# Kernel tuning notes

Measured on AMD Instinct MI355X. Metric: run time of the kernel, lower is better.

## Reference

```python
import jax, jax.numpy as jnp
import numpy as np

N_NODES = 100000
N_EDGES = 1600000


def setup_inputs() -> dict:
    key = jax.random.key(0)
    ks = jax.random.split(key, 6)
    x = jax.random.normal(ks[0], (N_NODES, 128), dtype=jnp.float32)
    src = jax.random.randint(ks[1], (N_EDGES,), 0, N_NODES, dtype=jnp.int32)
    dst = jax.random.randint(ks[2], (N_EDGES,), 0, N_NODES, dtype=jnp.int32)
    # Glorot-ish scaled weights
    W1 = jax.random.normal(ks[3], (128, 64), dtype=jnp.float32) / np.sqrt(128.0)
    b1 = jnp.zeros((64,), dtype=jnp.float32)
    W2 = jax.random.normal(ks[4], (64, 64), dtype=jnp.float32) / np.sqrt(64.0)
    b2 = jnp.zeros((64,), dtype=jnp.float32)
    return {"x": x, "src": src, "dst": dst, "W1": W1, "b1": b1, "W2": W2, "b2": b2}


def _gcn_forward(x, src_f, dst_f, norm_src, norm_dst, W1, b1, W2, b2):
    n = x.shape[0]

    def conv(h, W, b):
        # weight-first (in_feats >= out_feats in DGL GraphConv): h W is cheap, aggregate small dim
        h = h @ W                                  # [N, d_out]
        h = h * norm_src[:, None]                  # D_out^{-1/2} on source side
        msg = h[src_f]                             # gather per edge [E+N, d_out]
        agg = jax.ops.segment_sum(msg, dst_f, num_segments=n)  # scatter-add to dst
        return agg * norm_dst[:, None] + b         # D_in^{-1/2} + bias

    h = jax.nn.relu(conv(x, W1, b1))
    return conv(h, W2, b2)


def reference(x, src, dst, W1, b1, W2, b2):
    n = x.shape[0]
    loop = jnp.arange(n, dtype=src.dtype)
    src_f = jnp.concatenate([src, loop])  # dgl.add_self_loop
    dst_f = jnp.concatenate([dst, loop])
    ones = jnp.ones(src_f.shape[0], dtype=x.dtype)
    out_deg = jax.ops.segment_sum(ones, src_f, num_segments=n)
    in_deg = jax.ops.segment_sum(ones, dst_f, num_segments=n)
    norm_src = jax.lax.rsqrt(out_deg)  # deg >= 1 due to self loops
    norm_dst = jax.lax.rsqrt(in_deg)
    return _gcn_forward(x, src_f, dst_f, norm_src, norm_dst, W1, b1, W2, b2)
```

## Files before the change

kernel.cpp:

```cpp
#include <hip/hip_runtime.h>
#include <hip/hip_fp16.h>

#define D 64
#define SLICE 25000
#define NBUCK 512
#define EPB 4096

typedef __attribute__((ext_vector_type(8))) short short8;
typedef __attribute__((ext_vector_type(4))) float floatx4;

__global__ __launch_bounds__(256) void k_hist(const int* __restrict__ src,
                                              const int* __restrict__ dst,
                                              int* __restrict__ cnt_out,
                                              int* __restrict__ cnt_in,
                                              int E, int N) {
    __shared__ int h[SLICE];
    const int* idx = blockIdx.z ? dst : src;
    int* cnt       = blockIdx.z ? cnt_in : cnt_out;
    int lo = blockIdx.y * SLICE;
    int hi = min(lo + SLICE, N);
    int len = hi - lo;
    for (int i = threadIdx.x; i < len; i += 256) h[i] = 0;
    __syncthreads();

    const int E4 = E >> 2;
    const int4* idx4 = (const int4*)idx;
    int stride = gridDim.x * 256;
    for (int i = blockIdx.x * 256 + threadIdx.x; i < E4; i += stride) {
        int4 v = idx4[i];
        if (v.x >= lo && v.x < hi) atomicAdd(&h[v.x - lo], 1);
        if (v.y >= lo && v.y < hi) atomicAdd(&h[v.y - lo], 1);
        if (v.z >= lo && v.z < hi) atomicAdd(&h[v.z - lo], 1);
        if (v.w >= lo && v.w < hi) atomicAdd(&h[v.w - lo], 1);
    }
    if (blockIdx.x == 0) {
        int e = E4 * 4 + threadIdx.x;
        if (e < E) {
            int v = idx[e];
            if (v >= lo && v < hi) atomicAdd(&h[v - lo], 1);
        }
    }
    __syncthreads();
    for (int i = threadIdx.x; i < len; i += 256) {
        int c = h[i];
        if (c) atomicAdd(&cnt[lo + i], c);
    }
}

__global__ __launch_bounds__(256) void k_norm(const int* __restrict__ cnt,
                                              float* __restrict__ nrm, int n) {
    int i = blockIdx.x * 256 + threadIdx.x;
    if (i < n) nrm[i] = rsqrtf((float)cnt[i] + 1.0f);
}

__global__ __launch_bounds__(256) void k_scan1(const int* __restrict__ in,
                                               int* __restrict__ out,
                                               int* __restrict__ partials, int n) {
    __shared__ int s[256];
    int tid = threadIdx.x;
    int base = blockIdx.x * 1024 + tid * 4;
    int v[4];
#pragma unroll
    for (int j = 0; j < 4; ++j) v[j] = (base + j < n) ? in[base + j] : 0;
    int l1 = v[0] + v[1];
    int l2 = l1 + v[2];
    int total = l2 + v[3];
    s[tid] = total;
    __syncthreads();
    for (int off = 1; off < 256; off <<= 1) {
        int add = (tid >= off) ? s[tid - off] : 0;
        __syncthreads();
        s[tid] += add;
        __syncthreads();
    }
    int excl = s[tid] - total;
    if (base + 0 < n) out[base + 0] = excl;
    if (base + 1 < n) out[base + 1] = excl + v[0];
    if (base + 2 < n) out[base + 2] = excl + l1;
    if (base + 3 < n) out[base + 3] = excl + l2;
    if (tid == 255) partials[blockIdx.x] = s[255];
}

__global__ void k_scan2(int* __restrict__ partials, int B) {
    if (threadIdx.x == 0) {
        int run = 0;
        for (int i = 0; i < B; ++i) {
            int tmp = partials[i];
            partials[i] = run;
            run += tmp;
        }
    }
}

__global__ __launch_bounds__(256) void k_scan3(int* __restrict__ out,
                                               const int* __restrict__ partials, int n) {
    int off = partials[blockIdx.x];
    int base = blockIdx.x * 1024 + threadIdx.x * 4;
#pragma unroll
    for (int j = 0; j < 4; ++j)
        if (base + j < n) out[base + j] += off;
}

__global__ __launch_bounds__(256) void k_bhist(const int* __restrict__ dst,
                                               int* __restrict__ bucket_cnt, int E) {
    __shared__ int h[NBUCK];
    for (int i = threadIdx.x; i < NBUCK; i += 256) h[i] = 0;
    __syncthreads();
    const int E4 = E >> 2;
    const int4* d4 = (const int4*)dst;
    int stride = gridDim.x * 256;
    for (int i = blockIdx.x * 256 + threadIdx.x; i < E4; i += stride) {
        int4 v = d4[i];
        atomicAdd(&h[v.x >> 8], 1);
        atomicAdd(&h[v.y >> 8], 1);
        atomicAdd(&h[v.z >> 8], 1);
        atomicAdd(&h[v.w >> 8], 1);
    }
    if (blockIdx.x == 0) {
        int e = E4 * 4 + threadIdx.x;
        if (e < E) atomicAdd(&h[dst[e] >> 8], 1);
    }
    __syncthreads();
    for (int i = threadIdx.x; i < NBUCK; i += 256) {
        int c = h[i];
        if (c) atomicAdd(&bucket_cnt[i], c);
    }
}

__global__ __launch_bounds__(256) void k_bscan(const int* __restrict__ bucket_cnt,
                                               int* __restrict__ bucket_base) {
    __shared__ int s[256];
    int tid = threadIdx.x;
    int a = bucket_cnt[2 * tid];
    int b = bucket_cnt[2 * tid + 1];
    s[tid] = a + b;
    __syncthreads();
    for (int off = 1; off < 256; off <<= 1) {
        int add = (tid >= off) ? s[tid - off] : 0;
        __syncthreads();
        s[tid] += add;
        __syncthreads();
    }
    int excl = s[tid] - (a + b);
    bucket_base[2 * tid]     = excl;
    bucket_base[2 * tid + 1] = excl + a;
}

__global__ __launch_bounds__(256) void k_bin(const int* __restrict__ src,
                                             const int* __restrict__ dst,
                                             const int* __restrict__ bucket_base,
                                             int* __restrict__ bucket_cursor,
                                             unsigned long long* __restrict__ binned,
                                             int E) {
    __shared__ int cnt[NBUCK];
    __shared__ int bloc[NBUCK];
    __shared__ int lcur[NBUCK];
    __shared__ int gbase[NBUCK];
    __shared__ int ss[256];
    __shared__ unsigned long long stage[EPB];

    int tid = threadIdx.x;
    int start = blockIdx.x * EPB;
    int nloc = min(EPB, E - start);

    for (int i = tid; i < NBUCK; i += 256) cnt[i] = 0;
    __syncthreads();

#pragma unroll
    for (int r = 0; r < EPB / 256; ++r) {
        int idx = start + r * 256 + tid;
        if (idx < E) atomicAdd(&cnt[dst[idx] >> 8], 1);
    }
    __syncthreads();

    int a = cnt[2 * tid], b = cnt[2 * tid + 1];
    ss[tid] = a + b;
    __syncthreads();
    for (int off = 1; off < 256; off <<= 1) {
        int add = (tid >= off) ? ss[tid - off] : 0;
        __syncthreads();
        ss[tid] += add;
        __syncthreads();
    }
    int excl = ss[tid] - (a + b);
    bloc[2 * tid] = excl;           lcur[2 * tid] = excl;
    bloc[2 * tid + 1] = excl + a;   lcur[2 * tid + 1] = excl + a;
    __syncthreads();

    for (int bk = tid; bk < NBUCK; bk += 256) {
        int c = cnt[bk];
        gbase[bk] = c ? (atomicAdd(&bucket_cursor[bk], c) + bucket_base[bk]) : 0;
    }
    __syncthreads();

#pragma unroll
    for (int r = 0; r < EPB / 256; ++r) {
        int idx = start + r * 256 + tid;
        if (idx < E) {
            int d = dst[idx];
            int p = atomicAdd(&lcur[d >> 8], 1);
            stage[p] = ((unsigned long long)(unsigned)d << 32) | (unsigned)src[idx];
        }
    }
    __syncthreads();

#pragma unroll
    for (int r = 0; r < EPB / 256; ++r) {
        int i = r * 256 + tid;
        if (i < nloc) {
            unsigned long long e = stage[i];
            int bk = (int)(e >> 40);
            binned[gbase[bk] + (i - bloc[bk])] = e;
        }
    }
}

__global__ __launch_bounds__(256) void k_bsort(const unsigned long long* __restrict__ binned,
                                               const int* __restrict__ bucket_base,
                                               const int* __restrict__ bucket_cnt,
                                               const int* __restrict__ row_ptr,
                                               int* __restrict__ csr, int N) {
    __shared__ int cur[256];
    int b = blockIdx.x;
    int n0 = b << 8;
    int tid = threadIdx.x;
    if (n0 + tid < N) cur[tid] = row_ptr[n0 + tid];
    __syncthreads();
    int base = bucket_base[b];
    int c = bucket_cnt[b];
    for (int k = tid; k < c; k += 256) {
        unsigned long long e = binned[base + k];
        int d = (int)(e >> 32);
        int s = (int)(e & 0xffffffffu);
        int p = atomicAdd(&cur[d - n0], 1);
        csr[p] = s;
    }
}

template <int K>
__global__ __launch_bounds__(256) void k_gemm_mfma(const float* __restrict__ hsrc,
                                                   const float* __restrict__ W,
                                                   const float* __restrict__ norm_src,
                                                   __half* __restrict__ t, int N) {
    constexpr int NKI = K / 32;
    __shared__ short Whi[NKI * 2048];
    __shared__ short Wlo[NKI * 2048];
    int tid = threadIdx.x;

    for (int f = tid; f < K * 64; f += 256) {
        int n  = f & 15;
        int j  = (f >> 4) & 7;
        int q  = (f >> 7) & 3;
        int ct = (f >> 9) & 3;
        int ki = f >> 11;
        int k = ki * 32 + q * 8 + j;
        int c = ct * 16 + n;
        float w = W[k * 64 + c];
        unsigned u = __float_as_uint(w);
        float l = w - __uint_as_float(u & 0xffff0000u);
        int idx = (((ki * 4 + ct) * 16 + n) * 4 + q) * 8 + j;
        Whi[idx] = (short)(u >> 16);
        Wlo[idx] = (short)(__float_as_uint(l) >> 16);
    }
    __syncthreads();

    int wave = tid >> 6, lane = tid & 63;
    int q = lane >> 4, n = lane & 15;
    int r0 = blockIdx.x * 64 + wave * 16;
    int rowc = min(r0 + n, N - 1);

    floatx4 acc[4] = {{0.f,0.f,0.f,0.f},{0.f,0.f,0.f,0.f},
                      {0.f,0.f,0.f,0.f},{0.f,0.f,0.f,0.f}};

    for (int ki = 0; ki < NKI; ++ki) {
        const float* ap = hsrc + (long long)rowc * K + ki * 32 + q * 8;
        float4 a0 = *(const float4*)ap;
        float4 a1 = *(const float4*)(ap + 4);
        float av[8] = {a0.x, a0.y, a0.z, a0.w, a1.x, a1.y, a1.z, a1.w};
        short8 ahi, alo;
#pragma unroll
        for (int j = 0; j < 8; ++j) {
            unsigned u = __float_as_uint(av[j]);
            float l = av[j] - __uint_as_float(u & 0xffff0000u);
            ahi[j] = (short)(u >> 16);
            alo[j] = (short)(__float_as_uint(l) >> 16);
        }
#pragma unroll
        for (int ct = 0; ct < 4; ++ct) {
            int bidx = (((ki * 4 + ct) * 16 + n) * 4 + q) * 8;
            short8 bhi = *(const short8*)&Whi[bidx];
            short8 blo = *(const short8*)&Wlo[bidx];
            acc[ct] = __builtin_amdgcn_mfma_f32_16x16x32_bf16(ahi, bhi, acc[ct], 0, 0, 0);
            acc[ct] = __builtin_amdgcn_mfma_f32_16x16x32_bf16(ahi, blo, acc[ct], 0, 0, 0);
            acc[ct] = __builtin_amdgcn_mfma_f32_16x16x32_bf16(alo, bhi, acc[ct], 0, 0, 0);
        }
    }

#pragma unroll
    for (int reg = 0; reg < 4; ++reg) {
        int orow = r0 + q * 4 + reg;
        if (orow < N) {
            float nrm = norm_src[orow];
#pragma unroll
            for (int ct = 0; ct < 4; ++ct)
                t[(long long)orow * 64 + ct * 16 + n] = __float2half(acc[ct][reg] * nrm);
        }
    }
}

__global__ __launch_bounds__(256) void k_agg(const int* __restrict__ row_ptr,
                                             const int* __restrict__ cnt,
                                             const int* __restrict__ csr,
                                             const __half* __restrict__ t,
                                             const float* __restrict__ norm_dst,
                                             const float* __restrict__ bias,
                                             float* __restrict__ out, int N, int do_relu) {
    int tid = threadIdx.x;
    int half_id = tid >> 5;
    int lane = tid & 31;
    int i = blockIdx.x * 8 + half_id;
    if (i >= N) return;
    const __half2* t2 = (const __half2*)t;
    int start = row_ptr[i], c = cnt[i];

    __half2 self = t2[i * 32 + lane];
    float2 sf = __half22float2(self);
    float ax = sf.x, ay = sf.y;

    int j = 0;
    int pre = min(c, (4 - (start & 3)) & 3);
    for (; j < pre; ++j) {
        float2 f = __half22float2(t2[csr[start + j] * 32 + lane]);
        ax += f.x; ay += f.y;
    }
    for (; j + 4 <= c; j += 4) {
        int4 s4 = *(const int4*)&csr[start + j];
        float2 f0 = __half22float2(t2[s4.x * 32 + lane]);
        float2 f1 = __half22float2(t2[s4.y * 32 + lane]);
        float2 f2 = __half22float2(t2[s4.z * 32 + lane]);
        float2 f3 = __half22float2(t2[s4.w * 32 + lane]);
        ax += (f0.x + f1.x) + (f2.x + f3.x);
        ay += (f0.y + f1.y) + (f2.y + f3.y);
    }
    for (; j < c; ++j) {
        float2 f = __half22float2(t2[csr[start + j] * 32 + lane]);
        ax += f.x; ay += f.y;
    }

    float nrm = norm_dst[i];
    float2 bb = ((const float2*)bias)[lane];
    float vx = fmaf(ax, nrm, bb.x);
    float vy = fmaf(ay, nrm, bb.y);
    if (do_relu) { vx = fmaxf(vx, 0.f); vy = fmaxf(vy, 0.f); }
    float2 o; o.x = vx; o.y = vy;
    ((float2*)out)[i * 32 + lane] = o;
}

extern "C" void kernel_launch(void* const* d_in, const int* in_sizes, int n_in,
                              void* d_out, int out_size, void* d_ws, size_t ws_size,
                              hipStream_t stream) {
    const float* x   = (const float*)d_in[0];
    const int*   src = (const int*)d_in[1];
    const int*   dst = (const int*)d_in[2];
    const float* W1  = (const float*)d_in[3];
    const float* b1  = (const float*)d_in[4];
    const float* W2  = (const float*)d_in[5];
    const float* b2  = (const float*)d_in[6];
    float* out = (float*)d_out;

    const int N = in_sizes[0] / 128;
    const int E = in_sizes[1];

    int*   cnt_out  = (int*)d_ws;
    int*   cnt_in   = cnt_out + N;
    int*   unused0  = cnt_in + N;
    int*   row_ptr  = unused0 + N;
    int*   partials = row_ptr + N;
    float* norm_src = (float*)(partials + 1024);
    float* norm_dst = norm_src + N;
    float* tbase    = norm_dst + N;
    float* h        = tbase + (long long)N * D;
    int*   csr      = (int*)(h + (long long)N * D);
    int*   bucket_cnt    = csr + E;
    int*   bucket_cursor = bucket_cnt + NBUCK;
    int*   bucket_base   = bucket_cursor + NBUCK;
    __half* t_h = (__half*)tbase;
    unsigned long long* binned = (unsigned long long*)tbase;

    const int B = (N + 1023) / 1024;
    const int NS = (N + SLICE - 1) / SLICE;
    const int NB = (N + 255) / 256;
    const int NBK = (E + EPB - 1) / EPB;

    hipMemsetAsync(cnt_out, 0, (size_t)2 * N * sizeof(int), stream);
    hipMemsetAsync(bucket_cnt, 0, (size_t)2 * NBUCK * sizeof(int), stream);

    k_hist<<<dim3(32, NS, 2), 256, 0, stream>>>(src, dst, cnt_out, cnt_in, E, N);
    k_norm<<<(2 * N + 255) / 256, 256, 0, stream>>>(cnt_out, norm_src, 2 * N);

    k_scan1<<<B, 256, 0, stream>>>(cnt_in, row_ptr, partials, N);
    k_scan2<<<1, 64, 0, stream>>>(partials, B);
    k_scan3<<<B, 256, 0, stream>>>(row_ptr, partials, N);

    k_bhist<<<64, 256, 0, stream>>>(dst, bucket_cnt, E);
    k_bscan<<<1, 256, 0, stream>>>(bucket_cnt, bucket_base);
    k_bin<<<NBK, 256, 0, stream>>>(src, dst, bucket_base, bucket_cursor, binned, E);
    k_bsort<<<NB, 256, 0, stream>>>(binned, bucket_base, bucket_cnt, row_ptr, csr, N);

    k_gemm_mfma<128><<<(N + 63) / 64, 256, 0, stream>>>(x, W1, norm_src, t_h, N);
    k_agg<<<(N + 7) / 8, 256, 0, stream>>>(row_ptr, cnt_in, csr, t_h, norm_dst, b1, h, N, 1);

    k_gemm_mfma<64><<<(N + 63) / 64, 256, 0, stream>>>(h, W2, norm_src, t_h, N);
    k_agg<<<(N + 7) / 8, 256, 0, stream>>>(row_ptr, cnt_in, csr, t_h, norm_dst, b2, out, N, 0);
}
```

Baseline: 336.6 us.

## Split feature table into column panels and derive buckets from row_ptr

The GEMM output is now written as four 16-column panels, each N×16 in half precision, about 3.2MB per panel. Aggregation runs four passes, one per panel, with 8 lanes per node, so each pass's gathers hit a working set small enough to stay in L2/MALL instead of thrashing the whole 12.8MB table. Separately, the bucket histogram and bucket scan kernels are removed and bucket bases and counts are read from row_ptr[bucket*256], which saves two launches and a full pass over dst. In exchange the CSR indices and row metadata are re-read four times per layer, and each gather now fetches only 32 bytes per node row.

```diff
diff --git a/kernel.cpp b/kernel.cpp
--- a/kernel.cpp
+++ b/kernel.cpp
@@ -81,7 +81,8 @@
     if (tid == 255) partials[blockIdx.x] = s[255];
 }
 
-__global__ void k_scan2(int* __restrict__ partials, int B) {
+__global__ void k_scan2(int* __restrict__ partials, int B,
+                        int* __restrict__ row_ptr, int N, int E) {
     if (threadIdx.x == 0) {
         int run = 0;
         for (int i = 0; i < B; ++i) {
@@ -90,6 +91,7 @@
             run += tmp;
         }
     }
+    if (threadIdx.x == 1) row_ptr[N] = E;
 }
 
 __global__ __launch_bounds__(256) void k_scan3(int* __restrict__ out,
@@ -101,54 +103,9 @@
         if (base + j < n) out[base + j] += off;
 }
 
-__global__ __launch_bounds__(256) void k_bhist(const int* __restrict__ dst,
-                                               int* __restrict__ bucket_cnt, int E) {
-    __shared__ int h[NBUCK];
-    for (int i = threadIdx.x; i < NBUCK; i += 256) h[i] = 0;
-    __syncthreads();
-    const int E4 = E >> 2;
-    const int4* d4 = (const int4*)dst;
-    int stride = gridDim.x * 256;
-    for (int i = blockIdx.x * 256 + threadIdx.x; i < E4; i += stride) {
-        int4 v = d4[i];
-        atomicAdd(&h[v.x >> 8], 1);
-        atomicAdd(&h[v.y >> 8], 1);
-        atomicAdd(&h[v.z >> 8], 1);
-        atomicAdd(&h[v.w >> 8], 1);
-    }
-    if (blockIdx.x == 0) {
-        int e = E4 * 4 + threadIdx.x;
-        if (e < E) atomicAdd(&h[dst[e] >> 8], 1);
-    }
-    __syncthreads();
-    for (int i = threadIdx.x; i < NBUCK; i += 256) {
-        int c = h[i];
-        if (c) atomicAdd(&bucket_cnt[i], c);
-    }
-}
-
-__global__ __launch_bounds__(256) void k_bscan(const int* __restrict__ bucket_cnt,
-                                               int* __restrict__ bucket_base) {
-    __shared__ int s[256];
-    int tid = threadIdx.x;
-    int a = bucket_cnt[2 * tid];
-    int b = bucket_cnt[2 * tid + 1];
-    s[tid] = a + b;
-    __syncthreads();
-    for (int off = 1; off < 256; off <<= 1) {
-        int add = (tid >= off) ? s[tid - off] : 0;
-        __syncthreads();
-        s[tid] += add;
-        __syncthreads();
-    }
-    int excl = s[tid] - (a + b);
-    bucket_base[2 * tid]     = excl;
-    bucket_base[2 * tid + 1] = excl + a;
-}
-
 __global__ __launch_bounds__(256) void k_bin(const int* __restrict__ src,
                                              const int* __restrict__ dst,
-                                             const int* __restrict__ bucket_base,
+                                             const int* __restrict__ row_ptr,
                                              int* __restrict__ bucket_cursor,
                                              unsigned long long* __restrict__ binned,
                                              int E) {
@@ -189,7 +146,7 @@
 
     for (int bk = tid; bk < NBUCK; bk += 256) {
         int c = cnt[bk];
-        gbase[bk] = c ? (atomicAdd(&bucket_cursor[bk], c) + bucket_base[bk]) : 0;
+        gbase[bk] = c ? (atomicAdd(&bucket_cursor[bk], c) + row_ptr[bk << 8]) : 0;
     }
     __syncthreads();
 
@@ -216,8 +173,6 @@
 }
 
 __global__ __launch_bounds__(256) void k_bsort(const unsigned long long* __restrict__ binned,
-                                               const int* __restrict__ bucket_base,
-                                               const int* __restrict__ bucket_cnt,
                                                const int* __restrict__ row_ptr,
                                                int* __restrict__ csr, int N) {
     __shared__ int cur[256];
@@ -226,8 +181,8 @@
     int tid = threadIdx.x;
     if (n0 + tid < N) cur[tid] = row_ptr[n0 + tid];
     __syncthreads();
-    int base = bucket_base[b];
-    int c = bucket_cnt[b];
+    int base = row_ptr[n0];
+    int c = row_ptr[min(n0 + 256, N)] - base;
     for (int k = tid; k < c; k += 256) {
         unsigned long long e = binned[base + k];
         int d = (int)(e >> 32);
@@ -303,7 +258,7 @@
             float nrm = norm_src[orow];
 #pragma unroll
             for (int ct = 0; ct < 4; ++ct)
-                t[(long long)orow * 64 + ct * 16 + n] = __float2half(acc[ct][reg] * nrm);
+                t[(long long)ct * N * 16 + orow * 16 + n] = __float2half(acc[ct][reg] * nrm);
         }
     }
 }
@@ -311,49 +266,48 @@
 __global__ __launch_bounds__(256) void k_agg(const int* __restrict__ row_ptr,
                                              const int* __restrict__ cnt,
                                              const int* __restrict__ csr,
-                                             const __half* __restrict__ t,
+                                             const __half* __restrict__ tp,
                                              const float* __restrict__ norm_dst,
-                                             const float* __restrict__ bias,
-                                             float* __restrict__ out, int N, int do_relu) {
-    int tid = threadIdx.x;
-    int half_id = tid >> 5;
-    int lane = tid & 31;
-    int i = blockIdx.x * 8 + half_id;
+                                             const float* __restrict__ bias16,
+                                             float* __restrict__ outp,
+                                             int N, int do_relu) {
+    int tid = threadIdx.x;
+    int g = tid & 7;
+    int i = blockIdx.x * 32 + (tid >> 3);
     if (i >= N) return;
-    const __half2* t2 = (const __half2*)t;
+    const __half2* t2 = (const __half2*)tp;
     int start = row_ptr[i], c = cnt[i];
 
-    __half2 self = t2[i * 32 + lane];
-    float2 sf = __half22float2(self);
+    float2 sf = __half22float2(t2[i * 8 + g]);
     float ax = sf.x, ay = sf.y;
 
     int j = 0;
     int pre = min(c, (4 - (start & 3)) & 3);
     for (; j < pre; ++j) {
-        float2 f = __half22float2(t2[csr[start + j] * 32 + lane]);
+        float2 f = __half22float2(t2[csr[start + j] * 8 + g]);
         ax += f.x; ay += f.y;
     }
     for (; j + 4 <= c; j += 4) {
         int4 s4 = *(const int4*)&csr[start + j];
-        float2 f0 = __half22float2(t2[s4.x * 32 + lane]);
-        float2 f1 = __half22float2(t2[s4.y * 32 + lane]);
-        float2 f2 = __half22float2(t2[s4.z * 32 + lane]);
-        float2 f3 = __half22float2(t2[s4.w * 32 + lane]);
+        float2 f0 = __half22float2(t2[s4.x * 8 + g]);
+        float2 f1 = __half22float2(t2[s4.y * 8 + g]);
+        float2 f2 = __half22float2(t2[s4.z * 8 + g]);
+        float2 f3 = __half22float2(t2[s4.w * 8 + g]);
         ax += (f0.x + f1.x) + (f2.x + f3.x);
         ay += (f0.y + f1.y) + (f2.y + f3.y);
     }
     for (; j < c; ++j) {
-        float2 f = __half22float2(t2[csr[start + j] * 32 + lane]);
+        float2 f = __half22float2(t2[csr[start + j] * 8 + g]);
         ax += f.x; ay += f.y;
     }
 
     float nrm = norm_dst[i];
-    float2 bb = ((const float2*)bias)[lane];
+    float2 bb = ((const float2*)bias16)[g];
     float vx = fmaf(ax, nrm, bb.x);
     float vy = fmaf(ay, nrm, bb.y);
     if (do_relu) { vx = fmaxf(vx, 0.f); vy = fmaxf(vy, 0.f); }
     float2 o; o.x = vx; o.y = vy;
-    ((float2*)out)[i * 32 + lane] = o;
+    ((float2*)outp)[i * 32 + g] = o;
 }
 
 extern "C" void kernel_launch(void* const* d_in, const int* in_sizes, int n_in,
@@ -373,17 +327,14 @@
 
     int*   cnt_out  = (int*)d_ws;
     int*   cnt_in   = cnt_out + N;
-    int*   unused0  = cnt_in + N;
-    int*   row_ptr  = unused0 + N;
-    int*   partials = row_ptr + N;
+    int*   row_ptr  = cnt_in + N;
+    int*   partials = row_ptr + N + 1;
     float* norm_src = (float*)(partials + 1024);
     float* norm_dst = norm_src + N;
     float* tbase    = norm_dst + N;
     float* h        = tbase + (long long)N * D;
     int*   csr      = (int*)(h + (long long)N * D);
-    int*   bucket_cnt    = csr + E;
-    int*   bucket_cursor = bucket_cnt + NBUCK;
-    int*   bucket_base   = bucket_cursor + NBUCK;
+    int*   bucket_cursor = csr + E;
     __half* t_h = (__half*)tbase;
     unsigned long long* binned = (unsigned long long*)tbase;
 
@@ -391,25 +342,30 @@
     const int NS = (N + SLICE - 1) / SLICE;
     const int NB = (N + 255) / 256;
     const int NBK = (E + EPB - 1) / EPB;
+    const int AGG_GRID = (N + 31) / 32;
 
     hipMemsetAsync(cnt_out, 0, (size_t)2 * N * sizeof(int), stream);
-    hipMemsetAsync(bucket_cnt, 0, (size_t)2 * NBUCK * sizeof(int), stream);
+    hipMemsetAsync(bucket_cursor, 0, (size_t)NBUCK * sizeof(int), stream);
 
     k_hist<<<dim3(32, NS, 2), 256, 0, stream>>>(src, dst, cnt_out, cnt_in, E, N);
     k_norm<<<(2 * N + 255) / 256, 256, 0, stream>>>(cnt_out, norm_src, 2 * N);
 
     k_scan1<<<B, 256, 0, stream>>>(cnt_in, row_ptr, partials, N);
-    k_scan2<<<1, 64, 0, stream>>>(partials, B);
+    k_scan2<<<1, 64, 0, stream>>>(partials, B, row_ptr, N, E);
     k_scan3<<<B, 256, 0, stream>>>(row_ptr, partials, N);
 
-    k_bhist<<<64, 256, 0, stream>>>(dst, bucket_cnt, E);
-    k_bscan<<<1, 256, 0, stream>>>(bucket_cnt, bucket_base);
-    k_bin<<<NBK, 256, 0, stream>>>(src, dst, bucket_base, bucket_cursor, binned, E);
-    k_bsort<<<NB, 256, 0, stream>>>(binned, bucket_base, bucket_cnt, row_ptr, csr, N);
+    k_bin<<<NBK, 256, 0, stream>>>(src, dst, row_ptr, bucket_cursor, binned, E);
+    k_bsort<<<NB, 256, 0, stream>>>(binned, row_ptr, csr, N);
 
     k_gemm_mfma<128><<<(N + 63) / 64, 256, 0, stream>>>(x, W1, norm_src, t_h, N);
-    k_agg<<<(N + 7) / 8, 256, 0, stream>>>(row_ptr, cnt_in, csr, t_h, norm_dst, b1, h, N, 1);
+    for (int p = 0; p < 4; ++p)
+        k_agg<<<AGG_GRID, 256, 0, stream>>>(row_ptr, cnt_in, csr,
+                                            t_h + (long long)p * N * 16, norm_dst,
+                                            b1 + p * 16, h + p * 16, N, 1);
 
     k_gemm_mfma<64><<<(N + 63) / 64, 256, 0, stream>>>(h, W2, norm_src, t_h, N);
-    k_agg<<<(N + 7) / 8, 256, 0, stream>>>(row_ptr, cnt_in, csr, t_h, norm_dst, b2, out, N, 0);
-}
+    for (int p = 0; p < 4; ++p)
+        k_agg<<<AGG_GRID, 256, 0, stream>>>(row_ptr, cnt_in, csr,
+                                            t_h + (long long)p * N * 16, norm_dst,
+                                            b2 + p * 16, out + p * 16, N, 0);
+}
```

New measurement: 413.9 us. +23.0%, slower.
